# Performance work log

Measured on AMD Instinct MI355X. Metric: run time of the kernel, lower is better.

The kernel has to match this reference:

```python
import jax, jax.numpy as jnp
import numpy as np

N_TREE = 200
DEPTH = 3
N_LEAF = 2 ** (DEPTH + 1) - 1      # 15 internal decision nodes
N_LEAVES = N_LEAF + 1              # 16 leaves
N_NODE = 64
BATCH = 2048
D_FEAT = 512
LR = 0.01


def _leaf_paths(depth):
    """For each of the 2^(depth+1) leaves, the internal-node index and the
    left/right bit at every level (matches the tf.gather index construction:
    bit==0 -> take p, bit==1 -> take 1-p; children of node n are 2n+1, 2n+2)."""
    L = 2 ** (depth + 1)
    nodes = np.zeros((L, depth + 1), np.int32)
    bits = np.zeros((L, depth + 1), np.int32)
    for l in range(L):
        node = 0
        for d in range(depth + 1):
            bit = (l >> (depth - d)) & 1
            nodes[l, d] = node
            bits[l, d] = bit
            node = 2 * node + 1 + bit
    return nodes, bits

_NODES, _BITS = _leaf_paths(DEPTH)


def setup_inputs() -> dict:
    key = jax.random.key(0)
    ks = jax.random.split(key, 9)
    u = lambda k, s: jax.random.uniform(k, s, jnp.float32, -0.05, 0.05)  # keras 'uniform' init
    return {
        "x": jax.random.normal(ks[0], (BATCH, D_FEAT), jnp.float32),
        "y_true": jax.random.normal(ks[1], (BATCH, 1), jnp.float32),
        "w_t": u(ks[2], (N_TREE, D_FEAT, N_NODE)),
        "b_t": u(ks[3], (N_TREE, N_NODE)),
        "w_d": u(ks[4], (N_TREE, N_NODE, N_LEAF)),
        "b_d": u(ks[5], (N_TREE, N_LEAF)),
        "w_l": u(ks[6], (N_TREE, N_LEAVES)),
        "b_l": u(ks[7], (N_TREE,)),
        "f_0": jnp.full((1,), 0.5, jnp.float32),
    }


def reference(x, y_true, w_t, b_t, w_d, b_d, w_l, b_l, f_0):
    B = x.shape[0]
    # Batched per-tree small MLP (the 200-iteration Python loop in the original).
    # Dropout is identity at inference.
    h = jax.nn.relu(jnp.einsum('bd,tdn->tbn', x, w_t) + b_t[:, None, :])        # [T,B,N_NODE]
    p = jax.nn.sigmoid(jnp.einsum('tbn,tnl->tbl', h, w_d) + b_d[:, None, :])    # [T,B,15]
    # Soft binary-tree routing: mu[t,b,leaf] = prod over path of p or (1-p).
    # This reproduces the tiled-index tf.gather construction exactly.
    pn = p[..., _NODES]                                                         # [T,B,16,DEPTH+1]
    q = jnp.where(_BITS == 1, 1.0 - pn, pn)
    mu = jnp.prod(q, axis=-1)                                                   # [T,B,16]
    # Per-tree leaf score with tanh.
    f = jnp.tanh(jnp.einsum('tbl,tl->tb', mu, w_l) + b_l[:, None])              # [T,B]
    # Sequential boosting accumulation: predict_k = f_0 + lr * sum_{i<k} f_i.
    cum = f_0 + LR * jnp.cumsum(f.T, axis=1)                                    # [B,T]
    py_x = jnp.concatenate([jnp.broadcast_to(f_0[None, :], (B, 1)), cum], axis=1)  # [B,T+1]
    return py_x
```

## Files before the change

### kernel.cpp

```cpp
#include <hip/hip_runtime.h>

#define T_TREES 200
#define BATCH   2048
#define D_FEAT  512
#define N_NODE  64
#define LR      0.01f

typedef __attribute__((__ext_vector_type__(8)))  __bf16 bf16x8;
typedef __attribute__((__ext_vector_type__(16))) float  f32x16;

__device__ __forceinline__ unsigned short f32_to_bf16(float f) {
    unsigned u = __float_as_uint(f);
    u += 0x7FFFu + ((u >> 16) & 1u);
    return (unsigned short)(u >> 16);
}

__device__ __forceinline__ void gload_lds16(const void* g, void* l) {
    __builtin_amdgcn_global_load_lds(
        (__attribute__((address_space(1))) void*)(void*)g,
        (__attribute__((address_space(3))) void*)l,
        16, 0, 0);
}

__global__ __launch_bounds__(256) void prep_all(
    const float* __restrict__ x, const float* __restrict__ w_t,
    const float* __restrict__ w_d,
    unsigned short* __restrict__ x_p, unsigned short* __restrict__ w_p,
    unsigned short* __restrict__ w_dt) {
    __shared__ float tile[64 * 65];
    int b = blockIdx.x;
    if (b < 256) {
        int mb = b >> 3, slab = b & 7;
        const float* src = x + (mb * 64) * D_FEAT + slab * 64;
        #pragma unroll
        for (int p = 0; p < 16; ++p) {
            int idx = p * 256 + threadIdx.x;
            int r = idx >> 6, c = idx & 63;
            tile[r * 65 + c] = src[r * D_FEAT + c];
        }
        __syncthreads();
        int mt = mb >> 1, mq = mb & 1;
        unsigned short* dst = x_p + mt * 65536 + slab * 8192 + mq * 512;
        #pragma unroll
        for (int p = 0; p < 8; ++p) {
            int idx = p * 256 + threadIdx.x;
            int kgl = idx >> 8;
            int r   = (idx >> 2) & 63;
            int jp  = idx & 3;
            ushort2 o;
            o.x = f32_to_bf16(tile[r * 65 + kgl * 8 + jp * 2]);
            o.y = f32_to_bf16(tile[r * 65 + kgl * 8 + jp * 2 + 1]);
            *(ushort2*)(dst + kgl * 1024 + r * 8 + jp * 2) = o;
        }
    } else if (b < 1856) {
        int bb = b - 256;
        int t = bb >> 3, slab = bb & 7;
        const float* src = w_t + t * (D_FEAT * N_NODE) + slab * 64 * N_NODE;
        #pragma unroll
        for (int p = 0; p < 16; ++p) {
            int idx = p * 256 + threadIdx.x;
            int d = idx >> 6, n = idx & 63;
            tile[d * 65 + n] = src[d * N_NODE + n];
        }
        __syncthreads();
        unsigned short* dst = w_p + (t >> 1) * 65536 + slab * 8192 + (t & 1) * 512;
        #pragma unroll
        for (int p = 0; p < 8; ++p) {
            int idx = p * 256 + threadIdx.x;
            int kgl = idx >> 8;
            int n   = (idx >> 2) & 63;
            int jp  = idx & 3;
            ushort2 o;
            o.x = f32_to_bf16(tile[(kgl * 8 + jp * 2) * 65 + n]);
            o.y = f32_to_bf16(tile[(kgl * 8 + jp * 2 + 1) * 65 + n]);
            *(ushort2*)(dst + kgl * 1024 + n * 8 + jp * 2) = o;
        }
    } else {
        int i = (b - 1856) * 256 + threadIdx.x;
        int n = i & 63;
        int l = (i >> 6) & 31;
        int t = i >> 11;
        float v = (l < 15) ? w_d[(t * 64 + n) * 15 + l] : 0.f;
        w_dt[i] = f32_to_bf16(v);
    }
}

__global__ __launch_bounds__(256, 3) void gbdt_main(
    const unsigned short* __restrict__ x_p,
    const unsigned short* __restrict__ w_p,
    const unsigned short* __restrict__ w_dt,
    const float* __restrict__ b_t,
    const float* __restrict__ b_d,
    const float* __restrict__ w_l,
    const float* __restrict__ b_l,
    float* __restrict__ f_ws)
{
    __shared__ alignas(16) char smem[34816];
    unsigned short* Hs = (unsigned short*)smem;
    float*          Pf = (float*)smem;

    const int tid    = threadIdx.x;
    const int lane   = tid & 63;
    const int w      = tid >> 6;
    const int lane31 = lane & 31;
    const int kh     = lane >> 5;
    const int wm     = w >> 1;
    const int wn     = w & 1;

    const int xcd  = blockIdx.x & 7;
    const int slot = blockIdx.x >> 3;
    const int mt   = slot & 15;
    const int pj   = slot >> 4;
    const int pair = xcd * 13 + pj;
    if (pair >= 100) return;
    const int t0 = pair * 2;
    const int m0 = mt * 128;
    const int phase = slot & 7;

    const unsigned short* pA = x_p + mt * 65536 + kh * 1024 + (wm * 64 + lane31) * 8;
    const char* gb = (const char*)(w_p + pair * 65536) + tid * 16;

    f32x16 acc[2][2];
    #pragma unroll
    for (int mb = 0; mb < 2; ++mb)
        #pragma unroll
        for (int nb = 0; nb < 2; ++nb)
            acc[mb][nb] = (f32x16)(0.f);

    bf16x8 a_cur[8], a_nxt[8];
    {
        const unsigned short* pc = pA + phase * 8192;
        #pragma unroll
        for (int s2 = 0; s2 < 4; ++s2)
            #pragma unroll
            for (int mb = 0; mb < 2; ++mb)
                a_cur[s2 * 2 + mb] = *(const bf16x8*)(pc + s2 * 2048 + mb * 256);
        #pragma unroll
        for (int i = 0; i < 4; ++i)
            gload_lds16(gb + phase * 16384 + i * 4096, smem + tid * 16 + i * 4096);
    }

    #pragma unroll
    for (int c = 0; c < 8; ++c) {
        __syncthreads();
        if (c < 7) {
            const int cc = (c + 1 + phase) & 7;
            char* nx = smem + ((c + 1) & 1) * 16384;
            #pragma unroll
            for (int i = 0; i < 4; ++i)
                gload_lds16(gb + cc * 16384 + i * 4096, nx + tid * 16 + i * 4096);
            const unsigned short* pc = pA + cc * 8192;
            #pragma unroll
            for (int s2 = 0; s2 < 4; ++s2)
                #pragma unroll
                for (int mb = 0; mb < 2; ++mb)
                    a_nxt[s2 * 2 + mb] = *(const bf16x8*)(pc + s2 * 2048 + mb * 256);
        }
        const char* buf = smem + (c & 1) * 16384;
        #pragma unroll
        for (int s2 = 0; s2 < 4; ++s2) {
            const int kgl = 2 * s2 + kh;
            bf16x8 bv[2];
            #pragma unroll
            for (int nb = 0; nb < 2; ++nb)
                bv[nb] = *(const bf16x8*)(buf + (kgl * 128 + wn * 64 + nb * 32 + lane31) * 16);
            #pragma unroll
            for (int mb = 0; mb < 2; ++mb)
                #pragma unroll
                for (int nb = 0; nb < 2; ++nb)
                    acc[mb][nb] = __builtin_amdgcn_mfma_f32_32x32x16_bf16(
                        a_cur[s2 * 2 + mb], bv[nb], acc[mb][nb], 0, 0, 0);
        }
        #pragma unroll
        for (int i = 0; i < 8; ++i) a_cur[i] = a_nxt[i];
    }

    __syncthreads();

    #pragma unroll
    for (int nb = 0; nb < 2; ++nb) {
        float btv = b_t[(t0 + wn) * 64 + nb * 32 + lane31];
        #pragma unroll
        for (int mb = 0; mb < 2; ++mb)
            #pragma unroll
            for (int r = 0; r < 16; ++r) {
                int m = wm * 64 + mb * 32 + (r & 3) + 8 * (r >> 2) + 4 * kh;
                float h = fmaxf(acc[mb][nb][r] + btv, 0.f);
                Hs[wn * 8704 + m * 68 + nb * 32 + lane31] = f32_to_bf16(h);
            }
    }
    __syncthreads();

    f32x16 acc2[2] = { (f32x16)(0.f), (f32x16)(0.f) };
    const unsigned short* pW = w_dt + (t0 + wn) * 2048 + lane31 * 64 + kh * 8;
    #pragma unroll
    for (int s = 0; s < 4; ++s) {
        bf16x8 bv = *(const bf16x8*)(pW + s * 16);
        #pragma unroll
        for (int i = 0; i < 2; ++i) {
            const unsigned short* pH =
                Hs + wn * 8704 + (wm * 64 + i * 32 + lane31) * 68 + s * 16 + kh * 8;
            bf16x8 av = *(const bf16x8*)pH;
            acc2[i] = __builtin_amdgcn_mfma_f32_32x32x16_bf16(av, bv, acc2[i], 0, 0, 0);
        }
    }
    __syncthreads();

    if (lane31 < 15) {
        float bdv = b_d[(t0 + wn) * 15 + lane31];
        #pragma unroll
        for (int i = 0; i < 2; ++i)
            #pragma unroll
            for (int r = 0; r < 16; ++r) {
                int m = wm * 64 + i * 32 + (r & 3) + 8 * (r >> 2) + 4 * kh;
                float lg = acc2[i][r] + bdv;
                Pf[(wn * 128 + m) * 17 + lane31] = 1.f / (1.f + __expf(-lg));
            }
    }
    __syncthreads();

    {
        int m = tid & 127;
        int j = tid >> 7;
        int t = t0 + j;
        float pv[15];
        #pragma unroll
        for (int i = 0; i < 15; ++i) pv[i] = Pf[(j * 128 + m) * 17 + i];
        float facc = 0.f;
        #pragma unroll
        for (int leaf = 0; leaf < 16; ++leaf) {
            float mu = 1.f;
            int node = 0;
            #pragma unroll
            for (int d = 0; d < 4; ++d) {
                int bit = (leaf >> (3 - d)) & 1;
                float p = pv[node];
                mu *= bit ? (1.f - p) : p;
                node = 2 * node + 1 + bit;
            }
            facc += mu * w_l[t * 16 + leaf];
        }
        f_ws[(m0 + m) * T_TREES + t] = tanhf(facc + b_l[t]);
    }
}

__global__ void scan_k(const float* __restrict__ f_ws, const float* __restrict__ f0p,
                       float* __restrict__ out) {
    int b = blockIdx.x, tid = threadIdx.x;
    int lane = tid & 63, wid = tid >> 6;
    float f0 = f0p[0];
    float x = (tid < T_TREES) ? f_ws[b * T_TREES + tid] : 0.f;
    #pragma unroll
    for (int off = 1; off < 64; off <<= 1) {
        float y = __shfl_up(x, off, 64);
        if (lane >= off) x += y;
    }
    __shared__ float wsum[4];
    if (lane == 63) wsum[wid] = x;
    __syncthreads();
    float base = 0.f;
    for (int i = 0; i < wid; ++i) base += wsum[i];
    float incl = x + base;
    if (tid == 0) out[b * (T_TREES + 1)] = f0;
    if (tid < T_TREES) out[b * (T_TREES + 1) + 1 + tid] = f0 + LR * incl;
}

extern "C" void kernel_launch(void* const* d_in, const int* in_sizes, int n_in,
                              void* d_out, int out_size, void* d_ws, size_t ws_size,
                              hipStream_t stream) {
    const float* x   = (const float*)d_in[0];
    const float* w_t = (const float*)d_in[2];
    const float* b_t = (const float*)d_in[3];
    const float* w_d = (const float*)d_in[4];
    const float* b_d = (const float*)d_in[5];
    const float* w_l = (const float*)d_in[6];
    const float* b_l = (const float*)d_in[7];
    const float* f_0 = (const float*)d_in[8];
    float* out = (float*)d_out;

    char* ws = (char*)d_ws;
    unsigned short* x_p  = (unsigned short*)(ws);
    unsigned short* w_p  = (unsigned short*)(ws + 2097152);
    unsigned short* w_dt = (unsigned short*)(ws + 15204352);
    float*          f_ws = (float*)(ws + 16023552);

    prep_all<<<3456, 256, 0, stream>>>(x, w_t, w_d, x_p, w_p, w_dt);
    gbdt_main<<<1664, 256, 0, stream>>>(x_p, w_p, w_dt, b_t, b_d, w_l, b_l, f_ws);
    scan_k<<<BATCH, 256, 0, stream>>>(f_ws, f_0, out);
}
```

Measured before the change: 133.5 us.

## Retile main kernel to one tree per block with whole weight tile resident in LDS

Each block now handles one tree and 512 batch rows instead of a tree pair and 128 rows. The full 512x64 bf16 weight slice for the tree is loaded once into LDS (64KB), and each wave streams its own 128 rows of x from global memory with register double-buffering, using a 128x64 accumulator per wave. The aim is more reuse of the weight tile per block, fewer blocks (800 instead of 1664) and fewer barriers in the K loop. In exchange, LDS use per block doubles, occupancy drops to 2 blocks per CU, and x loads are no longer staged through shared memory, so each wave relies on register prefetch to hide global latency.

Result: no change. 134.2 us (+0.5%).

```diff
diff --git a/kernel.cpp b/kernel.cpp
--- a/kernel.cpp
+++ b/kernel.cpp
@@ -85,7 +85,7 @@
     }
 }
 
-__global__ __launch_bounds__(256, 3) void gbdt_main(
+__global__ __launch_bounds__(256, 2) void gbdt_main(
     const unsigned short* __restrict__ x_p,
     const unsigned short* __restrict__ w_p,
     const unsigned short* __restrict__ w_dt,
@@ -95,7 +95,7 @@
     const float* __restrict__ b_l,
     float* __restrict__ f_ws)
 {
-    __shared__ alignas(16) char smem[34816];
+    __shared__ alignas(16) char smem[69632];
     unsigned short* Hs = (unsigned short*)smem;
     float*          Pf = (float*)smem;
 
@@ -104,128 +104,134 @@
     const int w      = tid >> 6;
     const int lane31 = lane & 31;
     const int kh     = lane >> 5;
-    const int wm     = w >> 1;
-    const int wn     = w & 1;
 
     const int xcd  = blockIdx.x & 7;
     const int slot = blockIdx.x >> 3;
-    const int mt   = slot & 15;
-    const int pj   = slot >> 4;
-    const int pair = xcd * 13 + pj;
-    if (pair >= 100) return;
-    const int t0 = pair * 2;
-    const int m0 = mt * 128;
-    const int phase = slot & 7;
-
-    const unsigned short* pA = x_p + mt * 65536 + kh * 1024 + (wm * 64 + lane31) * 8;
-    const char* gb = (const char*)(w_p + pair * 65536) + tid * 16;
-
-    f32x16 acc[2][2];
-    #pragma unroll
-    for (int mb = 0; mb < 2; ++mb)
+    const int t    = xcd * 25 + (slot >> 2);
+    const int mt4  = slot & 3;
+    const int m0   = mt4 * 512;
+
+    {
+        const unsigned short* src =
+            w_p + (t >> 1) * 65536 + (t & 1) * 512 + (w * 64 + lane31 * 2 + kh) * 8;
+        #pragma unroll
+        for (int i = 0; i < 16; ++i) {
+            int kg = i * 4 + w;
+            gload_lds16(w_p + (t >> 1) * 65536 + kg * 1024 + (t & 1) * 512 + lane * 8,
+                        smem + kg * 1024 + lane * 16);
+        }
+        (void)src;
+    }
+
+    const unsigned short* pA =
+        x_p + (mt4 * 4 + w) * 65536 + kh * 1024 + lane31 * 8;
+
+    f32x16 acc[4][2];
+    #pragma unroll
+    for (int mb = 0; mb < 4; ++mb)
         #pragma unroll
         for (int nb = 0; nb < 2; ++nb)
             acc[mb][nb] = (f32x16)(0.f);
 
-    bf16x8 a_cur[8], a_nxt[8];
-    {
-        const unsigned short* pc = pA + phase * 8192;
-        #pragma unroll
-        for (int s2 = 0; s2 < 4; ++s2)
-            #pragma unroll
-            for (int mb = 0; mb < 2; ++mb)
-                a_cur[s2 * 2 + mb] = *(const bf16x8*)(pc + s2 * 2048 + mb * 256);
-        #pragma unroll
-        for (int i = 0; i < 4; ++i)
-            gload_lds16(gb + phase * 16384 + i * 4096, smem + tid * 16 + i * 4096);
-    }
-
-    #pragma unroll
-    for (int c = 0; c < 8; ++c) {
-        __syncthreads();
-        if (c < 7) {
-            const int cc = (c + 1 + phase) & 7;
-            char* nx = smem + ((c + 1) & 1) * 16384;
-            #pragma unroll
-            for (int i = 0; i < 4; ++i)
-                gload_lds16(gb + cc * 16384 + i * 4096, nx + tid * 16 + i * 4096);
-            const unsigned short* pc = pA + cc * 8192;
-            #pragma unroll
-            for (int s2 = 0; s2 < 4; ++s2)
-                #pragma unroll
-                for (int mb = 0; mb < 2; ++mb)
-                    a_nxt[s2 * 2 + mb] = *(const bf16x8*)(pc + s2 * 2048 + mb * 256);
-        }
-        const char* buf = smem + (c & 1) * 16384;
-        #pragma unroll
-        for (int s2 = 0; s2 < 4; ++s2) {
-            const int kgl = 2 * s2 + kh;
+    bf16x8 a0[4], a1[4];
+    #pragma unroll
+    for (int mb = 0; mb < 4; ++mb) {
+        a0[mb] = *(const bf16x8*)(pA + 0 * 2048 + mb * 256);
+        a1[mb] = *(const bf16x8*)(pA + 1 * 2048 + mb * 256);
+    }
+
+    __syncthreads();
+
+    #pragma unroll
+    for (int c = 0; c < 16; ++c) {
+        const int st0 = 2 * c, st1 = 2 * c + 1;
+        bf16x8 n0[4], n1[4];
+        #pragma unroll
+        for (int mb = 0; mb < 4; ++mb) {
+            n0[mb] = *(const bf16x8*)(pA + ((st0 + 2) & 31) * 2048 + mb * 256);
+            n1[mb] = *(const bf16x8*)(pA + ((st1 + 2) & 31) * 2048 + mb * 256);
+        }
+        {
             bf16x8 bv[2];
             #pragma unroll
             for (int nb = 0; nb < 2; ++nb)
-                bv[nb] = *(const bf16x8*)(buf + (kgl * 128 + wn * 64 + nb * 32 + lane31) * 16);
-            #pragma unroll
-            for (int mb = 0; mb < 2; ++mb)
+                bv[nb] = *(const bf16x8*)(smem + (2 * st0 + kh) * 1024 +
+                                          (nb * 32 + lane31) * 16);
+            #pragma unroll
+            for (int mb = 0; mb < 4; ++mb)
                 #pragma unroll
                 for (int nb = 0; nb < 2; ++nb)
                     acc[mb][nb] = __builtin_amdgcn_mfma_f32_32x32x16_bf16(
-                        a_cur[s2 * 2 + mb], bv[nb], acc[mb][nb], 0, 0, 0);
-        }
-        #pragma unroll
-        for (int i = 0; i < 8; ++i) a_cur[i] = a_nxt[i];
+                        a0[mb], bv[nb], acc[mb][nb], 0, 0, 0);
+        }
+        {
+            bf16x8 bv[2];
+            #pragma unroll
+            for (int nb = 0; nb < 2; ++nb)
+                bv[nb] = *(const bf16x8*)(smem + (2 * st1 + kh) * 1024 +
+                                          (nb * 32 + lane31) * 16);
+            #pragma unroll
+            for (int mb = 0; mb < 4; ++mb)
+                #pragma unroll
+                for (int nb = 0; nb < 2; ++nb)
+                    acc[mb][nb] = __builtin_amdgcn_mfma_f32_32x32x16_bf16(
+                        a1[mb], bv[nb], acc[mb][nb], 0, 0, 0);
+        }
+        #pragma unroll
+        for (int mb = 0; mb < 4; ++mb) { a0[mb] = n0[mb]; a1[mb] = n1[mb]; }
     }
 
     __syncthreads();
 
     #pragma unroll
     for (int nb = 0; nb < 2; ++nb) {
-        float btv = b_t[(t0 + wn) * 64 + nb * 32 + lane31];
-        #pragma unroll
-        for (int mb = 0; mb < 2; ++mb)
+        float btv = b_t[t * 64 + nb * 32 + lane31];
+        #pragma unroll
+        for (int mb = 0; mb < 4; ++mb)
             #pragma unroll
             for (int r = 0; r < 16; ++r) {
-                int m = wm * 64 + mb * 32 + (r & 3) + 8 * (r >> 2) + 4 * kh;
+                int m = w * 128 + mb * 32 + (r & 3) + 8 * (r >> 2) + 4 * kh;
                 float h = fmaxf(acc[mb][nb][r] + btv, 0.f);
-                Hs[wn * 8704 + m * 68 + nb * 32 + lane31] = f32_to_bf16(h);
+                Hs[m * 68 + nb * 32 + lane31] = f32_to_bf16(h);
             }
     }
     __syncthreads();
 
-    f32x16 acc2[2] = { (f32x16)(0.f), (f32x16)(0.f) };
-    const unsigned short* pW = w_dt + (t0 + wn) * 2048 + lane31 * 64 + kh * 8;
+    f32x16 acc2[4];
+    #pragma unroll
+    for (int i = 0; i < 4; ++i) acc2[i] = (f32x16)(0.f);
+    const unsigned short* pW = w_dt + t * 2048 + lane31 * 64 + kh * 8;
     #pragma unroll
     for (int s = 0; s < 4; ++s) {
         bf16x8 bv = *(const bf16x8*)(pW + s * 16);
         #pragma unroll
-        for (int i = 0; i < 2; ++i) {
-            const unsigned short* pH =
-                Hs + wn * 8704 + (wm * 64 + i * 32 + lane31) * 68 + s * 16 + kh * 8;
-            bf16x8 av = *(const bf16x8*)pH;
+        for (int i = 0; i < 4; ++i) {
+            bf16x8 av = *(const bf16x8*)(Hs + (w * 128 + i * 32 + lane31) * 68 +
+                                         s * 16 + kh * 8);
             acc2[i] = __builtin_amdgcn_mfma_f32_32x32x16_bf16(av, bv, acc2[i], 0, 0, 0);
         }
     }
     __syncthreads();
 
     if (lane31 < 15) {
-        float bdv = b_d[(t0 + wn) * 15 + lane31];
-        #pragma unroll
-        for (int i = 0; i < 2; ++i)
+        float bdv = b_d[t * 15 + lane31];
+        #pragma unroll
+        for (int i = 0; i < 4; ++i)
             #pragma unroll
             for (int r = 0; r < 16; ++r) {
-                int m = wm * 64 + i * 32 + (r & 3) + 8 * (r >> 2) + 4 * kh;
+                int m = w * 128 + i * 32 + (r & 3) + 8 * (r >> 2) + 4 * kh;
                 float lg = acc2[i][r] + bdv;
-                Pf[(wn * 128 + m) * 17 + lane31] = 1.f / (1.f + __expf(-lg));
+                Pf[m * 17 + lane31] = 1.f / (1.f + __expf(-lg));
             }
     }
     __syncthreads();
 
-    {
-        int m = tid & 127;
-        int j = tid >> 7;
-        int t = t0 + j;
+    #pragma unroll
+    for (int h = 0; h < 2; ++h) {
+        int m = h * 256 + tid;
         float pv[15];
         #pragma unroll
-        for (int i = 0; i < 15; ++i) pv[i] = Pf[(j * 128 + m) * 17 + i];
+        for (int i = 0; i < 15; ++i) pv[i] = Pf[m * 17 + i];
         float facc = 0.f;
         #pragma unroll
         for (int leaf = 0; leaf < 16; ++leaf) {
@@ -285,6 +291,6 @@
     float*          f_ws = (float*)(ws + 16023552);
 
     prep_all<<<3456, 256, 0, stream>>>(x, w_t, w_d, x_p, w_p, w_dt);
-    gbdt_main<<<1664, 256, 0, stream>>>(x_p, w_p, w_dt, b_t, b_d, w_l, b_l, f_ws);
+    gbdt_main<<<800, 256, 0, stream>>>(x_p, w_p, w_dt, b_t, b_d, w_l, b_l, f_ws);
     scan_k<<<BATCH, 256, 0, stream>>>(f_ws, f_0, out);
 }
```
